# Performance work log

Measured on AMD Instinct MI355X. Metric: run time of the kernel, lower is better.

The kernel has to match this reference:

```python
import jax, jax.numpy as jnp
import numpy as np


def setup_inputs() -> dict:
    key = jax.random.key(0)
    k1, k2 = jax.random.split(key)
    B, H, W, D, K = 32, 64, 64, 64, 512
    inputs = jax.random.normal(k1, (B, H, W, D), dtype=jnp.float32)
    # codebook: (D, K) as in the keras layer (embedding_dim x num_embeddings)
    embeddings = jax.random.uniform(k2, (D, K), dtype=jnp.float32,
                                    minval=-1.0, maxval=1.0) * (3.0 / D) ** 0.5
    return {"inputs": inputs, "embeddings": embeddings}


def reference(inputs, embeddings):
    # inputs: [B, H, W, D]; embeddings: [D, K]
    D = inputs.shape[-1]
    flat = inputs.reshape(-1, D)                                   # [N, D]
    distances = (jnp.sum(flat * flat, axis=1, keepdims=True)
                 - 2.0 * (flat @ embeddings)
                 + jnp.sum(embeddings * embeddings, axis=0, keepdims=True))
    encoding_indices = jnp.argmin(distances, axis=1)               # [N]
    encoding_indices = encoding_indices.reshape(inputs.shape[:-1])  # [B, H, W]
    quantized = jnp.take(embeddings.T, encoding_indices, axis=0)   # [B, H, W, D]
    # straight-through estimator
    return inputs + jax.lax.stop_gradient(quantized - inputs)
```

## Files before the change

### kernel.cpp

```cpp
#include <hip/hip_runtime.h>


#define KC 512
#define DD 64
#define TAU 5e-4f

typedef __attribute__((ext_vector_type(8))) short short8;
typedef __attribute__((ext_vector_type(4))) float float4v;

__device__ inline unsigned short f2bf(float f) {
    unsigned u = __float_as_uint(f);
    return (unsigned short)((u + 0x7FFF + ((u >> 16) & 1)) >> 16);
}
__device__ inline float bf2f(unsigned short b) {
    return __uint_as_float((unsigned)b << 16);
}

__global__ __launch_bounds__(256) void vq_prep(const float* __restrict__ emb,
                                               float* __restrict__ et,
                                               float* __restrict__ bias,
                                               short* __restrict__ Bh,
                                               short* __restrict__ Bl) {
    __shared__ float tile[DD][17];
    const int ct = blockIdx.x;
    const int t  = threadIdx.x;

    {
        const int d = t >> 2, c0 = (t & 3) * 4;
        float4 v = *(const float4*)(emb + (size_t)d * KC + ct * 16 + c0);
        tile[d][c0 + 0] = v.x; tile[d][c0 + 1] = v.y;
        tile[d][c0 + 2] = v.z; tile[d][c0 + 3] = v.w;
    }
    __syncthreads();

    if (t < 16) {
        float s = 0.f;
        #pragma unroll
        for (int d = 0; d < DD; ++d) { float v = tile[d][t]; s += v * v; }
        bias[ct * 16 + t] = s;
    }

    {
        const int c = t >> 4, d0 = (t & 15) * 4;
        float4 v;
        v.x = tile[d0 + 0][c]; v.y = tile[d0 + 1][c];
        v.z = tile[d0 + 2][c]; v.w = tile[d0 + 3][c];
        *(float4*)(et + (size_t)(ct * 16 + c) * DD + d0) = v;
    }

    {
        const int term = t >> 7;
        const int kc   = (t >> 6) & 1;
        const int l    = t & 63;
        const int c    = l & 15, dq = l >> 4;
        short v8[8];
        #pragma unroll
        for (int j = 0; j < 8; ++j) {
            float f = tile[kc * 32 + dq * 8 + j][c];
            unsigned short h = f2bf(f);
            v8[j] = (short)(term == 0 ? h : f2bf(f - bf2f(h)));
        }
        short* dst = (term == 0 ? Bh : Bl) + ((size_t)(ct * 2 + kc) * 64 + l) * 8;
        *(short8*)dst = *(short8*)v8;
    }
}

__global__ __launch_bounds__(256) void vq_main(const float* __restrict__ x_in,
                                               const short* __restrict__ Bh,
                                               const short* __restrict__ Bl,
                                               const float* __restrict__ bias,
                                               const float* __restrict__ et,
                                               float* __restrict__ out) {
    __shared__ float bias_s[KC];
    __shared__ int   k1s[128];
    __shared__ float gaps[128];

    const int t = threadIdx.x, w = t >> 6, l = t & 63;
    const int col = l & 15, quad = l >> 4;
    const int R0 = blockIdx.x * 128;

    {
        float2 b2 = *(const float2*)(bias + 2 * t);
        bias_s[2 * t + 0] = b2.x; bias_s[2 * t + 1] = b2.y;
    }

    short8 ah[2][2], al[2][2];
    #pragma unroll
    for (int rt = 0; rt < 2; ++rt)
        #pragma unroll
        for (int kc = 0; kc < 2; ++kc) {
            const float* xp = x_in + (size_t)(R0 + w * 32 + rt * 16 + col) * DD
                            + kc * 32 + quad * 8;
            float4 xa = *(const float4*)xp;
            float4 xb = *(const float4*)(xp + 4);
            float f[8] = {xa.x, xa.y, xa.z, xa.w, xb.x, xb.y, xb.z, xb.w};
            #pragma unroll
            for (int j = 0; j < 8; ++j) {
                unsigned short h = f2bf(f[j]);
                ah[rt][kc][j] = (short)h;
                al[rt][kc][j] = (short)f2bf(f[j] - bf2f(h));
            }
        }
    __syncthreads();

    float v1[2][4], v2[2][4];
    int   k1[2][4];
    #pragma unroll
    for (int rt = 0; rt < 2; ++rt)
        #pragma unroll
        for (int r = 0; r < 4; ++r) {
            v1[rt][r] = 3.4e38f; v2[rt][r] = 3.4e38f; k1[rt][r] = 0;
        }

    #pragma unroll 2
    for (int ct = 0; ct < 32; ++ct) {
        short8 bh0 = *(const short8*)(Bh + ((size_t)(ct * 2 + 0) * 64 + l) * 8);
        short8 bh1 = *(const short8*)(Bh + ((size_t)(ct * 2 + 1) * 64 + l) * 8);
        short8 bl0 = *(const short8*)(Bl + ((size_t)(ct * 2 + 0) * 64 + l) * 8);
        short8 bl1 = *(const short8*)(Bl + ((size_t)(ct * 2 + 1) * 64 + l) * 8);
        float bs = bias_s[ct * 16 + col];
        const int kk = ct * 16 + col;
        #pragma unroll
        for (int rt = 0; rt < 2; ++rt) {
            float4v c = {0.f, 0.f, 0.f, 0.f};
            c = __builtin_amdgcn_mfma_f32_16x16x32_bf16(ah[rt][0], bh0, c, 0, 0, 0);
            c = __builtin_amdgcn_mfma_f32_16x16x32_bf16(ah[rt][1], bh1, c, 0, 0, 0);
            c = __builtin_amdgcn_mfma_f32_16x16x32_bf16(al[rt][0], bh0, c, 0, 0, 0);
            c = __builtin_amdgcn_mfma_f32_16x16x32_bf16(al[rt][1], bh1, c, 0, 0, 0);
            c = __builtin_amdgcn_mfma_f32_16x16x32_bf16(ah[rt][0], bl0, c, 0, 0, 0);
            c = __builtin_amdgcn_mfma_f32_16x16x32_bf16(ah[rt][1], bl1, c, 0, 0, 0);
            #pragma unroll
            for (int r = 0; r < 4; ++r) {
                float s = fmaf(c[r], -2.0f, bs);
                bool lt = s < v1[rt][r];
                v2[rt][r] = lt ? v1[rt][r] : fminf(v2[rt][r], s);
                k1[rt][r] = lt ? kk : k1[rt][r];
                v1[rt][r] = lt ? s : v1[rt][r];
            }
        }
    }

    #pragma unroll
    for (int rt = 0; rt < 2; ++rt)
        #pragma unroll
        for (int r = 0; r < 4; ++r) {
            float bv1 = v1[rt][r], bv2 = v2[rt][r];
            int   bk  = k1[rt][r];
            #pragma unroll
            for (int m = 1; m <= 8; m <<= 1) {
                float ov1 = __shfl_xor(bv1, m, 64);
                float ov2 = __shfl_xor(bv2, m, 64);
                int   ok  = __shfl_xor(bk,  m, 64);
                float nv2 = fminf(fminf(bv2, ov2), fmaxf(bv1, ov1));
                bool take = (ov1 < bv1) || (ov1 == bv1 && ok < bk);
                bv1 = take ? ov1 : bv1;
                bk  = take ? ok  : bk;
                bv2 = nv2;
            }
            if (col == 0) {
                int row_l = w * 32 + rt * 16 + quad * 4 + r;
                k1s[row_l]  = bk;
                gaps[row_l] = bv2 - bv1;
            }
        }

    for (int rr = 0; rr < 32; ++rr) {
        const int row_l = w * 32 + rr;
        if (gaps[row_l] <= TAU) {
            const size_t grow = (size_t)(R0 + row_l) * DD;
            const int kbase = l * 8;
            float acc[8];
            #pragma unroll
            for (int j = 0; j < 8; ++j) acc[j] = 0.f;
            for (int d0 = 0; d0 < DD; d0 += 4) {
                float4 xv = *(const float4*)(x_in + grow + d0);
                #pragma unroll
                for (int j = 0; j < 8; ++j) {
                    float4 ev = *(const float4*)(et + (size_t)(kbase + j) * DD + d0);
                    acc[j] += xv.x * ev.x;
                    acc[j] += xv.y * ev.y;
                    acc[j] += xv.z * ev.z;
                    acc[j] += xv.w * ev.w;
                }
            }
            float4 b0 = *(const float4*)(bias + kbase);
            float4 b1 = *(const float4*)(bias + kbase + 4);
            float bb[8] = {b0.x, b0.y, b0.z, b0.w, b1.x, b1.y, b1.z, b1.w};
            float bv = 3.4e38f; int bk = 0;
            #pragma unroll
            for (int j = 0; j < 8; ++j) {
                float s = bb[j] - 2.f * acc[j];
                if (s < bv) { bv = s; bk = kbase + j; }
            }
            #pragma unroll
            for (int m = 1; m <= 32; m <<= 1) {
                float ov = __shfl_xor(bv, m, 64);
                int   ok = __shfl_xor(bk, m, 64);
                if (ov < bv || (ov == bv && ok < bk)) { bv = ov; bk = ok; }
            }
            if (l == 0) k1s[row_l] = bk;
        }
    }
    __syncthreads();

    {
        const int row_l = t >> 1, half = t & 1;
        const int bk = k1s[row_l];
        const float4* qp = (const float4*)(et + (size_t)bk * DD + half * 32);
        float4* op = (float4*)(out + (size_t)(R0 + row_l) * DD + half * 32);
        #pragma unroll
        for (int i = 0; i < 8; ++i) op[i] = qp[i];
    }
}

extern "C" void kernel_launch(void* const* d_in, const int* in_sizes, int n_in,
                              void* d_out, int out_size, void* d_ws, size_t ws_size,
                              hipStream_t stream) {
    const float* x_in = (const float*)d_in[0];
    const float* emb  = (const float*)d_in[1];
    float* out = (float*)d_out;

    float* et   = (float*)d_ws;
    float* bias = et + KC * DD;
    short* Bh   = (short*)(bias + KC);
    short* Bl   = Bh + 32 * 2 * 64 * 8;

    const int N = out_size / DD;

    vq_prep<<<32, 256, 0, stream>>>(emb, et, bias, Bh, Bl);
    vq_main<<<N / 128, 256, 0, stream>>>(x_in, Bh, Bl, bias, et, out);
}
```

Baseline: 135.7 us.

## Pack distance and index into sortable uint, double rows per block, prefetch codebook

Each wave now handles 64 rows (RT=4) instead of 32, so every loaded codebook fragment is reused across twice as many MFMAs. Codebook fragments are double-buffered in registers to overlap loads with compute, and the MFMA chains are split into two interleaved accumulators. The top-2 tracking packs a positive-shifted distance (bias + 64) with the 9-bit index into one unsigned integer, so plain integer min/max replaces compares and selects. The packing truncates mantissa bits, so the fallback threshold TAU is raised; this may send more rows through the slow fp32 rescoring path, and the larger register footprint may reduce occupancy.

After: 205.1 us. 1.51x slower.

```diff
diff --git a/kernel.cpp b/kernel.cpp
--- a/kernel.cpp
+++ b/kernel.cpp
@@ -3,7 +3,8 @@
 
 #define KC 512
 #define DD 64
-#define TAU 5e-4f
+#define RT 4
+#define TAU 0.008f
 
 typedef __attribute__((ext_vector_type(8))) short short8;
 typedef __attribute__((ext_vector_type(4))) float float4v;
@@ -15,10 +16,12 @@
 __device__ inline float bf2f(unsigned short b) {
     return __uint_as_float((unsigned)b << 16);
 }
+__device__ inline unsigned umin_u(unsigned a, unsigned b) { return a < b ? a : b; }
+__device__ inline unsigned umax_u(unsigned a, unsigned b) { return a > b ? a : b; }
 
 __global__ __launch_bounds__(256) void vq_prep(const float* __restrict__ emb,
                                                float* __restrict__ et,
-                                               float* __restrict__ bias,
+                                               float* __restrict__ bias64,
                                                short* __restrict__ Bh,
                                                short* __restrict__ Bl) {
     __shared__ float tile[DD][17];
@@ -37,7 +40,7 @@
         float s = 0.f;
         #pragma unroll
         for (int d = 0; d < DD; ++d) { float v = tile[d][t]; s += v * v; }
-        bias[ct * 16 + t] = s;
+        bias64[ct * 16 + t] = s + 64.0f;
     }
 
     {
@@ -65,31 +68,32 @@
     }
 }
 
-__global__ __launch_bounds__(256) void vq_main(const float* __restrict__ x_in,
-                                               const short* __restrict__ Bh,
-                                               const short* __restrict__ Bl,
-                                               const float* __restrict__ bias,
-                                               const float* __restrict__ et,
-                                               float* __restrict__ out) {
-    __shared__ float bias_s[KC];
-    __shared__ int   k1s[128];
-    __shared__ float gaps[128];
+__global__ __launch_bounds__(256, 2) void vq_main(const float* __restrict__ x_in,
+                                                  const short* __restrict__ Bh,
+                                                  const short* __restrict__ Bl,
+                                                  const float* __restrict__ bias64,
+                                                  const float* __restrict__ et,
+                                                  float* __restrict__ out) {
+    __shared__ float b64s[KC];
+    __shared__ int   k1s[256];
+    __shared__ float gaps[256];
 
     const int t = threadIdx.x, w = t >> 6, l = t & 63;
     const int col = l & 15, quad = l >> 4;
-    const int R0 = blockIdx.x * 128;
-
-    {
-        float2 b2 = *(const float2*)(bias + 2 * t);
-        bias_s[2 * t + 0] = b2.x; bias_s[2 * t + 1] = b2.y;
-    }
-
-    short8 ah[2][2], al[2][2];
+    const int R0 = blockIdx.x * 256;
+    const int rowbase = R0 + w * 64;
+
+    {
+        float2 b2 = *(const float2*)(bias64 + 2 * t);
+        b64s[2 * t + 0] = b2.x; b64s[2 * t + 1] = b2.y;
+    }
+
+    short8 ah[RT][2], al[RT][2];
     #pragma unroll
-    for (int rt = 0; rt < 2; ++rt)
+    for (int rt = 0; rt < RT; ++rt)
         #pragma unroll
         for (int kc = 0; kc < 2; ++kc) {
-            const float* xp = x_in + (size_t)(R0 + w * 32 + rt * 16 + col) * DD
+            const float* xp = x_in + (size_t)(rowbase + rt * 16 + col) * DD
                             + kc * 32 + quad * 8;
             float4 xa = *(const float4*)xp;
             float4 xb = *(const float4*)(xp + 4);
@@ -103,69 +107,85 @@
         }
     __syncthreads();
 
-    float v1[2][4], v2[2][4];
-    int   k1[2][4];
+    unsigned v1[RT][4], v2[RT][4];
     #pragma unroll
-    for (int rt = 0; rt < 2; ++rt)
-        #pragma unroll
-        for (int r = 0; r < 4; ++r) {
-            v1[rt][r] = 3.4e38f; v2[rt][r] = 3.4e38f; k1[rt][r] = 0;
-        }
+    for (int rt = 0; rt < RT; ++rt)
+        #pragma unroll
+        for (int r = 0; r < 4; ++r) { v1[rt][r] = 0xFFFFFFFFu; v2[rt][r] = 0xFFFFFFFFu; }
+
+    const short8* Bh8 = (const short8*)Bh;
+    const short8* Bl8 = (const short8*)Bl;
+
+    short8 bb[2][4];
+    bb[0][0] = Bh8[(size_t)0 * 64 + l];
+    bb[0][1] = Bh8[(size_t)1 * 64 + l];
+    bb[0][2] = Bl8[(size_t)0 * 64 + l];
+    bb[0][3] = Bl8[(size_t)1 * 64 + l];
 
     #pragma unroll 2
     for (int ct = 0; ct < 32; ++ct) {
-        short8 bh0 = *(const short8*)(Bh + ((size_t)(ct * 2 + 0) * 64 + l) * 8);
-        short8 bh1 = *(const short8*)(Bh + ((size_t)(ct * 2 + 1) * 64 + l) * 8);
-        short8 bl0 = *(const short8*)(Bl + ((size_t)(ct * 2 + 0) * 64 + l) * 8);
-        short8 bl1 = *(const short8*)(Bl + ((size_t)(ct * 2 + 1) * 64 + l) * 8);
-        float bs = bias_s[ct * 16 + col];
-        const int kk = ct * 16 + col;
-        #pragma unroll
-        for (int rt = 0; rt < 2; ++rt) {
-            float4v c = {0.f, 0.f, 0.f, 0.f};
-            c = __builtin_amdgcn_mfma_f32_16x16x32_bf16(ah[rt][0], bh0, c, 0, 0, 0);
-            c = __builtin_amdgcn_mfma_f32_16x16x32_bf16(ah[rt][1], bh1, c, 0, 0, 0);
-            c = __builtin_amdgcn_mfma_f32_16x16x32_bf16(al[rt][0], bh0, c, 0, 0, 0);
-            c = __builtin_amdgcn_mfma_f32_16x16x32_bf16(al[rt][1], bh1, c, 0, 0, 0);
-            c = __builtin_amdgcn_mfma_f32_16x16x32_bf16(ah[rt][0], bl0, c, 0, 0, 0);
-            c = __builtin_amdgcn_mfma_f32_16x16x32_bf16(ah[rt][1], bl1, c, 0, 0, 0);
+        const int cur = ct & 1, nx = cur ^ 1;
+        if (ct < 31) {
+            bb[nx][0] = Bh8[(size_t)((ct + 1) * 2 + 0) * 64 + l];
+            bb[nx][1] = Bh8[(size_t)((ct + 1) * 2 + 1) * 64 + l];
+            bb[nx][2] = Bl8[(size_t)((ct + 1) * 2 + 0) * 64 + l];
+            bb[nx][3] = Bl8[(size_t)((ct + 1) * 2 + 1) * 64 + l];
+        }
+        const float    bs = b64s[ct * 16 + col];
+        const unsigned kk = (unsigned)(ct * 16 + col);
+
+        float4v c0[RT], c1[RT];
+        #pragma unroll
+        for (int rt = 0; rt < RT; ++rt) {
+            float4v z = {0.f, 0.f, 0.f, 0.f};
+            c0[rt] = __builtin_amdgcn_mfma_f32_16x16x32_bf16(ah[rt][0], bb[cur][0], z, 0, 0, 0);
+            c1[rt] = __builtin_amdgcn_mfma_f32_16x16x32_bf16(ah[rt][1], bb[cur][1], z, 0, 0, 0);
+        }
+        #pragma unroll
+        for (int rt = 0; rt < RT; ++rt) {
+            c0[rt] = __builtin_amdgcn_mfma_f32_16x16x32_bf16(al[rt][0], bb[cur][0], c0[rt], 0, 0, 0);
+            c1[rt] = __builtin_amdgcn_mfma_f32_16x16x32_bf16(al[rt][1], bb[cur][1], c1[rt], 0, 0, 0);
+        }
+        #pragma unroll
+        for (int rt = 0; rt < RT; ++rt) {
+            c0[rt] = __builtin_amdgcn_mfma_f32_16x16x32_bf16(ah[rt][0], bb[cur][2], c0[rt], 0, 0, 0);
+            c1[rt] = __builtin_amdgcn_mfma_f32_16x16x32_bf16(ah[rt][1], bb[cur][3], c1[rt], 0, 0, 0);
+        }
+        #pragma unroll
+        for (int rt = 0; rt < RT; ++rt) {
             #pragma unroll
             for (int r = 0; r < 4; ++r) {
-                float s = fmaf(c[r], -2.0f, bs);
-                bool lt = s < v1[rt][r];
-                v2[rt][r] = lt ? v1[rt][r] : fminf(v2[rt][r], s);
-                k1[rt][r] = lt ? kk : k1[rt][r];
-                v1[rt][r] = lt ? s : v1[rt][r];
+                float s = fmaf(c0[rt][r] + c1[rt][r], -2.0f, bs);
+                unsigned p = (__float_as_uint(s) & 0xFFFFFE00u) | kk;
+                v2[rt][r] = umax_u(v1[rt][r], umin_u(v2[rt][r], p));
+                v1[rt][r] = umin_u(v1[rt][r], p);
             }
         }
     }
 
     #pragma unroll
-    for (int rt = 0; rt < 2; ++rt)
+    for (int rt = 0; rt < RT; ++rt)
         #pragma unroll
         for (int r = 0; r < 4; ++r) {
-            float bv1 = v1[rt][r], bv2 = v2[rt][r];
-            int   bk  = k1[rt][r];
+            unsigned a1 = v1[rt][r], a2 = v2[rt][r];
             #pragma unroll
             for (int m = 1; m <= 8; m <<= 1) {
-                float ov1 = __shfl_xor(bv1, m, 64);
-                float ov2 = __shfl_xor(bv2, m, 64);
-                int   ok  = __shfl_xor(bk,  m, 64);
-                float nv2 = fminf(fminf(bv2, ov2), fmaxf(bv1, ov1));
-                bool take = (ov1 < bv1) || (ov1 == bv1 && ok < bk);
-                bv1 = take ? ov1 : bv1;
-                bk  = take ? ok  : bk;
-                bv2 = nv2;
+                unsigned o1 = (unsigned)__shfl_xor((int)a1, m, 64);
+                unsigned o2 = (unsigned)__shfl_xor((int)a2, m, 64);
+                a2 = umin_u(umin_u(a2, o2), umax_u(a1, o1));
+                a1 = umin_u(a1, o1);
             }
             if (col == 0) {
-                int row_l = w * 32 + rt * 16 + quad * 4 + r;
-                k1s[row_l]  = bk;
-                gaps[row_l] = bv2 - bv1;
-            }
-        }
-
-    for (int rr = 0; rr < 32; ++rr) {
-        const int row_l = w * 32 + rr;
+                const int row_l = w * 64 + rt * 16 + quad * 4 + r;
+                k1s[row_l]  = (int)(a1 & 511u);
+                float f1 = __uint_as_float(a1 & 0xFFFFFE00u);
+                float f2 = __uint_as_float(a2 & 0xFFFFFE00u);
+                gaps[row_l] = f2 - f1;
+            }
+        }
+
+    for (int rr = 0; rr < 64; ++rr) {
+        const int row_l = w * 64 + rr;
         if (gaps[row_l] <= TAU) {
             const size_t grow = (size_t)(R0 + row_l) * DD;
             const int kbase = l * 8;
@@ -183,13 +203,13 @@
                     acc[j] += xv.w * ev.w;
                 }
             }
-            float4 b0 = *(const float4*)(bias + kbase);
-            float4 b1 = *(const float4*)(bias + kbase + 4);
-            float bb[8] = {b0.x, b0.y, b0.z, b0.w, b1.x, b1.y, b1.z, b1.w};
+            float4 b0 = *(const float4*)(bias64 + kbase);
+            float4 b1 = *(const float4*)(bias64 + kbase + 4);
+            float bbv[8] = {b0.x, b0.y, b0.z, b0.w, b1.x, b1.y, b1.z, b1.w};
             float bv = 3.4e38f; int bk = 0;
             #pragma unroll
             for (int j = 0; j < 8; ++j) {
-                float s = bb[j] - 2.f * acc[j];
+                float s = bbv[j] - 2.f * acc[j];
                 if (s < bv) { bv = s; bk = kbase + j; }
             }
             #pragma unroll
@@ -204,12 +224,16 @@
     __syncthreads();
 
     {
-        const int row_l = t >> 1, half = t & 1;
-        const int bk = k1s[row_l];
-        const float4* qp = (const float4*)(et + (size_t)bk * DD + half * 32);
-        float4* op = (float4*)(out + (size_t)(R0 + row_l) * DD + half * 32);
-        #pragma unroll
-        for (int i = 0; i < 8; ++i) op[i] = qp[i];
+        const int r = t >> 2, seg = t & 3;
+        #pragma unroll
+        for (int i = 0; i < 4; ++i) {
+            const int row_l = i * 64 + r;
+            const int bk = k1s[row_l];
+            const float4* qp = (const float4*)(et + (size_t)bk * DD + seg * 16);
+            float4* op = (float4*)(out + (size_t)(R0 + row_l) * DD + seg * 16);
+            #pragma unroll
+            for (int i4 = 0; i4 < 4; ++i4) op[i4] = qp[i4];
+        }
     }
 }
 
@@ -220,13 +244,13 @@
     const float* emb  = (const float*)d_in[1];
     float* out = (float*)d_out;
 
-    float* et   = (float*)d_ws;
-    float* bias = et + KC * DD;
-    short* Bh   = (short*)(bias + KC);
-    short* Bl   = Bh + 32 * 2 * 64 * 8;
+    float* et     = (float*)d_ws;
+    float* bias64 = et + KC * DD;
+    short* Bh     = (short*)(bias64 + KC);
+    short* Bl     = Bh + 32 * 2 * 64 * 8;
 
     const int N = out_size / DD;
 
-    vq_prep<<<32, 256, 0, stream>>>(emb, et, bias, Bh, Bl);
-    vq_main<<<N / 128, 256, 0, stream>>>(x_in, Bh, Bl, bias, et, out);
-}
+    vq_prep<<<32, 256, 0, stream>>>(emb, et, bias64, Bh, Bl);
+    vq_main<<<N / 256, 256, 0, stream>>>(x_in, Bh, Bl, bias64, et, out);
+}
```
